# Kernel tuning notes

Hardware: AMD Instinct MI355X
Metric: run time of the kernel (lower is better)

## Reference

```python
import jax, jax.numpy as jnp
import numpy as np
import math

# Model hyperparameters (SchNet defaults)
H = 128        # hidden_channels
F = 128        # num_filters
G = 50         # num_gaussians
CUT = 6.0      # cutoff (Angstrom)
L_INT = 3      # num_interactions
# Graph scale
N_MOL = 512    # molecules
APM = 32       # atoms per molecule
N = N_MOL * APM
BOX = 10.0     # side of cubic box per molecule


def _ssp(x):
    # ShiftedSoftplus
    return jax.nn.softplus(x) - math.log(2.0)


def setup_inputs() -> dict:
    rng = np.random.default_rng(0)
    pos = rng.uniform(0.0, BOX, (N_MOL, APM, 3)).astype(np.float32)
    # radius graph within each molecule (faithful to radius_graph_custom,
    # precomputed here because edge count is data-dependent)
    srcs, dsts = [], []
    for m in range(N_MOL):
        p = pos[m]
        dm = np.linalg.norm(p[:, None, :] - p[None, :, :], axis=-1)
        mask = dm <= CUT
        np.fill_diagonal(mask, False)
        s, t = np.nonzero(mask)
        srcs.append(s + m * APM)
        dsts.append(t + m * APM)
    edge_index = np.stack([np.concatenate(srcs), np.concatenate(dsts)]).astype(np.int32)
    pos = pos.reshape(N, 3)
    batch = np.repeat(np.arange(N_MOL, dtype=np.int32), APM)
    z = rng.integers(1, 100, N).astype(np.int32)

    key = jax.random.key(0)
    ks = jax.random.split(key, 16)
    s = 0.1
    nrm = lambda k, shp: (jax.random.normal(k, shp, dtype=jnp.float32) * s)
    return {
        "z": jnp.asarray(z),
        "pos": jnp.asarray(pos),
        "batch": jnp.asarray(batch),
        "edge_index": jnp.asarray(edge_index),
        "emb": nrm(ks[0], (100, H)),
        "mlp_w1": nrm(ks[1], (L_INT, G, F)),
        "mlp_b1": jnp.zeros((L_INT, F), jnp.float32),
        "mlp_w2": nrm(ks[2], (L_INT, F, F)),
        "mlp_b2": jnp.zeros((L_INT, F), jnp.float32),
        "cf1_w": nrm(ks[3], (L_INT, H, F)),
        "cf2_w": nrm(ks[4], (L_INT, F, H)),
        "cf2_b": jnp.zeros((L_INT, H), jnp.float32),
        "lin_w": nrm(ks[5], (L_INT, H, H)),
        "lin_b": jnp.zeros((L_INT, H), jnp.float32),
        "out1_w": nrm(ks[6], (H, H // 2)),
        "out1_b": jnp.zeros((H // 2,), jnp.float32),
        "out2_w": nrm(ks[7], (H // 2, 1)),
        "out2_b": jnp.zeros((1,), jnp.float32),
    }


def reference(z, pos, batch, edge_index, emb,
              mlp_w1, mlp_b1, mlp_w2, mlp_b2,
              cf1_w, cf2_w, cf2_b, lin_w, lin_b,
              out1_w, out1_b, out2_w, out2_b):
    src, dst = edge_index[0], edge_index[1]
    # edge_weight = euclidean distance (== cdist[src, dst])
    d = jnp.sqrt(jnp.sum((pos[src] - pos[dst]) ** 2, axis=-1))  # [E]
    # GaussianSmearing
    offs = jnp.linspace(0.0, CUT, G)
    coeff = -0.5 / (CUT / (G - 1)) ** 2
    edge_attr = jnp.exp(coeff * (d[:, None] - offs[None, :]) ** 2)  # [E, G]
    # cosine cutoff
    Ccut = 0.5 * (jnp.cos(d * math.pi / CUT) + 1.0)  # [E]

    h = emb[z]  # [N, H]
    for l in range(L_INT):
        # edge filter MLP with cutoff
        W = _ssp(edge_attr @ mlp_w1[l] + mlp_b1[l]) @ mlp_w2[l] + mlp_b2[l]  # [E, F]
        W = W * Ccut[:, None]
        # CFConv: lin1 -> gather x_j -> multiply -> scatter-add to dst -> lin2
        msg = (h @ cf1_w[l])[src] * W                                # [E, F]
        agg = jax.ops.segment_sum(msg, dst, num_segments=N)          # [N, F]
        v = agg @ cf2_w[l] + cf2_b[l]                                # [N, H]
        v = _ssp(v)
        v = v @ lin_w[l] + lin_b[l]
        h = h + v  # residual

    h = _ssp(h @ out1_w + out1_b)
    h = h @ out2_w + out2_b                                          # [N, 1]
    out = jax.ops.segment_sum(h, batch, num_segments=N_MOL)          # [N_MOL, 1]
    return out
```

## Files before the change

### kernel.cpp

```cpp
#include <hip/hip_runtime.h>
#include <hip/hip_bf16.h>
#include <math.h>

#define NATOMS 16384
#define NMOL   512
#define APM    32
#define GDIM   50
#define KTAB   4096

#define STRH 132
#define STRA 136

typedef __attribute__((ext_vector_type(8))) short   short8;
typedef __attribute__((ext_vector_type(4))) float   floatx4;

__device__ __forceinline__ float ssp(float x) {
    float e = __expf(-fabsf(x));
    return fmaxf(x, 0.0f) + __logf(1.0f + e) - 0.69314718055994531f;
}

__device__ __forceinline__ unsigned short f2bf(float x) {
    union { float f; unsigned int u; } v; v.f = x;
    unsigned int lsb = (v.u >> 16) & 1u;
    v.u += 0x7fffu + lsb;
    return (unsigned short)(v.u >> 16);
}

__device__ __forceinline__ unsigned int pk2bf(float a, float b) {
    __hip_bfloat162 h = __float22bfloat162_rn(make_float2(a, b));
    unsigned int u;
    __builtin_memcpy(&u, &h, 4);
    return u;
}

#define KW1 72
#define KW2 136
#define NTILE (KTAB / 64)

__global__ __launch_bounds__(256) void mega_setup_kernel(
    const float* __restrict__ pos, const int* __restrict__ eidx, int E, int EB,
    int* __restrict__ rowptr,
    const float* __restrict__ cf1, const float* __restrict__ cf2,
    const float* __restrict__ lin, const float* __restrict__ out1,
    unsigned short* __restrict__ Wtall, unsigned int* __restrict__ meta,
    const float* __restrict__ w1_, const float* __restrict__ b1_,
    const float* __restrict__ w2_, const float* __restrict__ b2_,
    unsigned short* __restrict__ Tt)
{
    const int WB = (9 * 16384 + 64 * 128 + 255) / 256;
    const int b = blockIdx.x;
    const int tid = threadIdx.x;

    if (b < EB) {
        int idx = b * 256 + tid;
        if (idx < E) {
            int s = eidx[idx], t = eidx[E + idx];
            float dx = pos[3 * s]     - pos[3 * t];
            float dy = pos[3 * s + 1] - pos[3 * t + 1];
            float dz = pos[3 * s + 2] - pos[3 * t + 2];
            float d  = sqrtf(dx * dx + dy * dy + dz * dz);
            float u  = d * (float)(KTAB - 1) / 6.0f;
            int i = min((int)(u + 0.5f), KTAB - 1);
            meta[idx] = ((unsigned)i << 10) | ((unsigned)(s & 31) << 5) | (unsigned)(t & 31);
        } else if (idx < E + NATOMS + 1) {
            int a = idx - E;
            int lo = 0, hi = E;
            while (lo < hi) { int mid = (lo + hi) >> 1; if (eidx[mid] < a) lo = mid + 1; else hi = mid; }
            rowptr[a] = lo;
        } else if (idx < E + NATOMS + 1 + 3 * 128) {
            int q = idx - (E + NATOMS + 1);
            int l = q >> 7, f = q & 127;
            Tt[(size_t)l * (KTAB + 1) * 128 + (size_t)KTAB * 128 + f] = 0;
        }
        return;
    }
    if (b < EB + WB) {
        int idx = (b - EB) * 256 + tid;
        if (idx < 9 * 16384) {
            int wi = idx >> 14, rem = idx & 16383;
            int n = rem >> 7, k = rem & 127;
            int l = wi / 3, which = wi % 3;
            const float* src = (which == 0) ? cf1 : (which == 1) ? cf2 : lin;
            Wtall[idx] = f2bf(src[(size_t)l * 16384 + k * 128 + n]);
        } else if (idx < 9 * 16384 + 64 * 128) {
            int q = idx - 9 * 16384;
            int n = q >> 7, k = q & 127;
            Wtall[idx] = f2bf(out1[k * 64 + n]);
        }
        return;
    }

    __shared__ unsigned short s_bufA[128 * KW2];
    __shared__ unsigned short s_bufB[128 * KW1];

    const int tt = b - EB - WB;
    const int l  = tt / NTILE;
    const int bx = tt % NTILE;
    const float* w1 = w1_ + (size_t)l * GDIM * 128;
    const float* b1 = b1_ + (size_t)l * 128;
    const float* w2 = w2_ + (size_t)l * 128 * 128;
    const float* b2 = b2_ + (size_t)l * 128;
    unsigned short* Tg = Tt + (size_t)l * (KTAB + 1) * 128;

    unsigned short* s_w1T = s_bufB;
    unsigned short* s_w2T = s_bufA;
    unsigned short* s_t   = s_bufB;

    for (int i = tid; i < GDIM * 128; i += 256) {
        int g = i >> 7, f = i & 127;
        s_w1T[f * KW1 + g] = f2bf(w1[i]);
    }
    for (int i = tid; i < (64 - GDIM) * 128; i += 256) {
        int g = GDIM + (i >> 7), f = i & 127;
        s_w1T[f * KW1 + g] = 0;
    }
    for (int i = tid; i < 128 * 128; i += 256) {
        int k = i >> 7, n = i & 127;
        s_w2T[n * KW2 + k] = f2bf(w2[i]);
    }

    const int lane = tid & 63;
    const int w    = tid >> 6;
    const int l15  = lane & 15;
    const int quad = lane >> 4;

    float b1v[8], b2v[8];
    #pragma unroll
    for (int nt = 0; nt < 8; nt++) {
        b1v[nt] = b1[nt * 16 + l15];
        b2v[nt] = b2[nt * 16 + l15];
    }
    __syncthreads();

    const float hstep = 6.0f / (float)(KTAB - 1);
    const float step  = 6.0f / 49.0f;
    const float coeff = -0.5f / (step * step);
    const float pioc  = 3.14159265358979323846f / 6.0f;
    const int k0 = bx * 64;
    const float dm = (float)(k0 + w * 16 + l15) * hstep;

    floatx4 acc1[8];
    #pragma unroll
    for (int nt = 0; nt < 8; nt++) acc1[nt] = (floatx4){0.f, 0.f, 0.f, 0.f};
    #pragma unroll
    for (int ks = 0; ks < 2; ks++) {
        unsigned int ap[4];
        #pragma unroll
        for (int jj = 0; jj < 4; jj++) {
            int g0 = ks * 32 + quad * 8 + 2 * jj;
            float d0 = dm - (float)g0 * step;
            float d1 = dm - (float)(g0 + 1) * step;
            float v0 = (g0 < GDIM)     ? __expf(coeff * d0 * d0) : 0.0f;
            float v1 = (g0 + 1 < GDIM) ? __expf(coeff * d1 * d1) : 0.0f;
            ap[jj] = pk2bf(v0, v1);
        }
        short8 af;
        __builtin_memcpy(&af, ap, 16);
        #pragma unroll
        for (int nt = 0; nt < 8; nt++) {
            short8 bfg = *(const short8*)&s_w1T[(nt * 16 + l15) * KW1 + ks * 32 + quad * 8];
            acc1[nt] = __builtin_amdgcn_mfma_f32_16x16x32_bf16(af, bfg, acc1[nt], 0, 0, 0);
        }
    }
    __syncthreads();

    #pragma unroll
    for (int nt = 0; nt < 8; nt++) {
        #pragma unroll
        for (int r = 0; r < 4; r++) {
            int row = w * 16 + quad * 4 + r;
            s_t[row * KW2 + nt * 16 + l15] = f2bf(ssp(acc1[nt][r] + b1v[nt]));
        }
    }

    floatx4 acc2[8];
    #pragma unroll
    for (int nt = 0; nt < 8; nt++) acc2[nt] = (floatx4){0.f, 0.f, 0.f, 0.f};
    #pragma unroll
    for (int ks = 0; ks < 4; ks++) {
        short8 af = *(const short8*)&s_t[(w * 16 + l15) * KW2 + ks * 32 + quad * 8];
        #pragma unroll
        for (int nt = 0; nt < 8; nt++) {
            short8 bfg = *(const short8*)&s_w2T[(nt * 16 + l15) * KW2 + ks * 32 + quad * 8];
            acc2[nt] = __builtin_amdgcn_mfma_f32_16x16x32_bf16(af, bfg, acc2[nt], 0, 0, 0);
        }
    }

    #pragma unroll
    for (int nt = 0; nt < 8; nt++) {
        #pragma unroll
        for (int r = 0; r < 4; r++) {
            int row = w * 16 + quad * 4 + r;
            float d = (float)(k0 + row) * hstep;
            float cut = 0.5f * (__cosf(d * pioc) + 1.0f);
            Tg[(size_t)(k0 + row) * 128 + nt * 16 + l15] = f2bf((acc2[nt][r] + b2v[nt]) * cut);
        }
    }
}

__global__ __launch_bounds__(512, 4) void fused_schnet_kernel(
    const int* __restrict__ z, const float* __restrict__ emb,
    const int* __restrict__ rowptr, const unsigned int* __restrict__ meta,
    const unsigned short* __restrict__ Tt,
    const unsigned short* __restrict__ Wtall,
    const float* __restrict__ cf2_b, const float* __restrict__ lin_b,
    const float* __restrict__ out1_b, const float* __restrict__ out2_w,
    const float* __restrict__ out2_b,
    float* __restrict__ out)
{
    __shared__ float s_h[32 * STRH];
    __shared__ float s_hx[32 * 128];
    __shared__ unsigned short s_agg[32 * STRA];
    __shared__ unsigned int s_ko[32 * 32];
    __shared__ float s_red;
    unsigned short* s_t = (unsigned short*)s_hx;

    const int tid  = threadIdx.x;
    const int lane = tid & 63;
    const int w    = tid >> 6;
    const int l15  = lane & 15;
    const int quad = lane >> 4;
    const int r16  = (w & 1) * 16;
    const int c32  = (w >> 1) * 32;
    const int B0   = blockIdx.x * 32;

    const int half = lane >> 5;
    const int l31  = lane & 31;
    const unsigned tOff = (unsigned)(l31 << 3);
    const unsigned hOff = (unsigned)(l31 << 4);

    for (int i = tid; i < 32 * 128; i += 512) {
        int row = i >> 7, col = i & 127;
        s_h[row * STRH + col] = emb[(size_t)z[B0 + row] * 128 + col];
    }
    if (tid == 0) s_red = 0.0f;
    for (int i = tid; i < 32 * 32; i += 512)
        s_ko[i] = (unsigned)(KTAB << 8);

    const int ebase = rowptr[B0];
    const int nE    = rowptr[B0 + 32] - ebase;

    __syncthreads();

    for (int i = tid; i < nE; i += 512) {
        unsigned q = meta[ebase + i];
        int dstA = q & 31, srcA = (q >> 5) & 31;
        s_ko[(dstA << 5) + ((srcA & 1) << 4) + (srcA >> 1)] = (q >> 10) << 8;
    }

    const unsigned short* WtO = Wtall + 9 * 16384;
    const char* hxB = (const char*)s_hx;

    for (int l = 0; l < 3; l++) {
        const unsigned short* W1 = Wtall + (size_t)(l * 3 + 0) * 16384;
        const unsigned short* W2 = Wtall + (size_t)(l * 3 + 1) * 16384;
        const unsigned short* W3 = Wtall + (size_t)(l * 3 + 2) * 16384;
        const char* TlB = (const char*)(Tt + (size_t)l * (KTAB + 1) * 128);

        __syncthreads();

        floatx4 acc[2];
        #pragma unroll
        for (int nt = 0; nt < 2; nt++) acc[nt] = (floatx4){0.f, 0.f, 0.f, 0.f};
        #pragma unroll
        for (int ks = 0; ks < 4; ks++) {
            const float* hp = &s_h[(r16 + l15) * STRH + ks * 32 + quad * 8];
            float4 xa = *(const float4*)hp;
            float4 xb = *(const float4*)(hp + 4);
            unsigned int ap[4];
            ap[0] = pk2bf(xa.x, xa.y); ap[1] = pk2bf(xa.z, xa.w);
            ap[2] = pk2bf(xb.x, xb.y); ap[3] = pk2bf(xb.z, xb.w);
            short8 af;
            __builtin_memcpy(&af, ap, 16);
            #pragma unroll
            for (int nt = 0; nt < 2; nt++) {
                short8 bfg = *(const short8*)&W1[(size_t)(c32 + nt * 16 + l15) * 128 + ks * 32 + quad * 8];
                acc[nt] = __builtin_amdgcn_mfma_f32_16x16x32_bf16(af, bfg, acc[nt], 0, 0, 0);
            }
        }
        #pragma unroll
        for (int nt = 0; nt < 2; nt++) {
            #pragma unroll
            for (int r = 0; r < 4; r++)
                s_hx[(r16 + quad * 4 + r) * 128 + c32 + nt * 16 + l15] = acc[nt][r];
        }

        __syncthreads();

        for (int al = 0; al < 4; al++) {
            const int atom = (w << 2) + al;
            const unsigned* ko = &s_ko[(atom << 5) + (half << 4)];
            uint4 k0 = *(const uint4*)&ko[0];
            uint4 k1 = *(const uint4*)&ko[4];
            uint4 k2 = *(const uint4*)&ko[8];
            uint4 k3 = *(const uint4*)&ko[12];
            const unsigned koff[16] = { k0.x, k0.y, k0.z, k0.w,
                                        k1.x, k1.y, k1.z, k1.w,
                                        k2.x, k2.y, k2.z, k2.w,
                                        k3.x, k3.y, k3.z, k3.w };
            float pa[4][4];
            #pragma unroll
            for (int j = 0; j < 4; j++) {
                #pragma unroll
                for (int c = 0; c < 4; c++) pa[j][c] = 0.0f;
            }
            #pragma unroll
            for (int stp = 0; stp < 16; stp++) {
                const int pr = (stp << 1) + half;
                uint2 tp = *(const uint2*)(TlB + (koff[stp] + tOff));
                float4 hv = *(const float4*)(hxB + (unsigned)(pr << 9) + hOff);
                const int j = stp & 3;
                pa[j][0] = fmaf(hv.x, __uint_as_float(tp.x << 16),         pa[j][0]);
                pa[j][1] = fmaf(hv.y, __uint_as_float(tp.x & 0xffff0000u), pa[j][1]);
                pa[j][2] = fmaf(hv.z, __uint_as_float(tp.y << 16),         pa[j][2]);
                pa[j][3] = fmaf(hv.w, __uint_as_float(tp.y & 0xffff0000u), pa[j][3]);
            }
            float c0 = (pa[0][0] + pa[1][0]) + (pa[2][0] + pa[3][0]);
            float c1 = (pa[0][1] + pa[1][1]) + (pa[2][1] + pa[3][1]);
            float c2 = (pa[0][2] + pa[1][2]) + (pa[2][2] + pa[3][2]);
            float c3 = (pa[0][3] + pa[1][3]) + (pa[2][3] + pa[3][3]);
            c0 += __shfl_xor(c0, 32);
            c1 += __shfl_xor(c1, 32);
            c2 += __shfl_xor(c2, 32);
            c3 += __shfl_xor(c3, 32);
            if (half == 0) {
                uint2 pk = make_uint2(pk2bf(c0, c1), pk2bf(c2, c3));
                *(uint2*)&s_agg[atom * STRA + (l31 << 2)] = pk;
            }
        }

        __syncthreads();

        float bva[2], bvb[2];
        #pragma unroll
        for (int nt = 0; nt < 2; nt++) {
            bva[nt] = cf2_b[l * 128 + c32 + nt * 16 + l15];
            bvb[nt] = lin_b[l * 128 + c32 + nt * 16 + l15];
        }
        #pragma unroll
        for (int nt = 0; nt < 2; nt++) acc[nt] = (floatx4){0.f, 0.f, 0.f, 0.f};
        #pragma unroll
        for (int ks = 0; ks < 4; ks++) {
            short8 af = *(const short8*)&s_agg[(r16 + l15) * STRA + ks * 32 + quad * 8];
            #pragma unroll
            for (int nt = 0; nt < 2; nt++) {
                short8 bfg = *(const short8*)&W2[(size_t)(c32 + nt * 16 + l15) * 128 + ks * 32 + quad * 8];
                acc[nt] = __builtin_amdgcn_mfma_f32_16x16x32_bf16(af, bfg, acc[nt], 0, 0, 0);
            }
        }
        #pragma unroll
        for (int nt = 0; nt < 2; nt++) {
            #pragma unroll
            for (int r = 0; r < 4; r++) {
                int row = r16 + quad * 4 + r;
                s_t[row * STRA + c32 + nt * 16 + l15] = f2bf(ssp(acc[nt][r] + bva[nt]));
            }
        }

        __syncthreads();

        #pragma unroll
        for (int nt = 0; nt < 2; nt++) acc[nt] = (floatx4){0.f, 0.f, 0.f, 0.f};
        #pragma unroll
        for (int ks = 0; ks < 4; ks++) {
            short8 af = *(const short8*)&s_t[(r16 + l15) * STRA + ks * 32 + quad * 8];
            #pragma unroll
            for (int nt = 0; nt < 2; nt++) {
                short8 bfg = *(const short8*)&W3[(size_t)(c32 + nt * 16 + l15) * 128 + ks * 32 + quad * 8];
                acc[nt] = __builtin_amdgcn_mfma_f32_16x16x32_bf16(af, bfg, acc[nt], 0, 0, 0);
            }
        }
        #pragma unroll
        for (int nt = 0; nt < 2; nt++) {
            #pragma unroll
            for (int r = 0; r < 4; r++) {
                int row = r16 + quad * 4 + r;
                s_h[row * STRH + c32 + nt * 16 + l15] += acc[nt][r] + bvb[nt];
            }
        }
    }

    __syncthreads();

    const int c16 = (w >> 1) * 16;
    floatx4 ha = (floatx4){0.f, 0.f, 0.f, 0.f};
    #pragma unroll
    for (int ks = 0; ks < 4; ks++) {
        const float* hp = &s_h[(r16 + l15) * STRH + ks * 32 + quad * 8];
        float4 xa = *(const float4*)hp;
        float4 xb = *(const float4*)(hp + 4);
        unsigned int ap[4];
        ap[0] = pk2bf(xa.x, xa.y); ap[1] = pk2bf(xa.z, xa.w);
        ap[2] = pk2bf(xb.x, xb.y); ap[3] = pk2bf(xb.z, xb.w);
        short8 af;
        __builtin_memcpy(&af, ap, 16);
        short8 bfg = *(const short8*)&WtO[(size_t)(c16 + l15) * 128 + ks * 32 + quad * 8];
        ha = __builtin_amdgcn_mfma_f32_16x16x32_bf16(af, bfg, ha, 0, 0, 0);
    }
    float part = 0.0f;
    {
        float b1o = out1_b[c16 + l15];
        float o2  = out2_w[c16 + l15];
        #pragma unroll
        for (int r = 0; r < 4; r++)
            part += ssp(ha[r] + b1o) * o2;
    }
    #pragma unroll
    for (int off = 32; off > 0; off >>= 1) part += __shfl_down(part, off);
    if (lane == 0) atomicAdd(&s_red, part);
    __syncthreads();
    if (tid == 0) out[blockIdx.x] = s_red + 32.0f * out2_b[0];
}

extern "C" void kernel_launch(void* const* d_in, const int* in_sizes, int n_in,
                              void* d_out, int out_size, void* d_ws, size_t ws_size,
                              hipStream_t stream)
{
    const int*   z      = (const int*)d_in[0];
    const float* pos    = (const float*)d_in[1];
    const int*   eidx   = (const int*)d_in[3];
    const float* emb    = (const float*)d_in[4];
    const float* mlp_w1 = (const float*)d_in[5];
    const float* mlp_b1 = (const float*)d_in[6];
    const float* mlp_w2 = (const float*)d_in[7];
    const float* mlp_b2 = (const float*)d_in[8];
    const float* cf1_w  = (const float*)d_in[9];
    const float* cf2_w  = (const float*)d_in[10];
    const float* cf2_b  = (const float*)d_in[11];
    const float* lin_w  = (const float*)d_in[12];
    const float* lin_b  = (const float*)d_in[13];
    const float* out1_w = (const float*)d_in[14];
    const float* out1_b = (const float*)d_in[15];
    const float* out2_w = (const float*)d_in[16];
    const float* out2_b = (const float*)d_in[17];
    const int E = in_sizes[3] / 2;

    char* p = (char*)d_ws;
    unsigned int* meta = (unsigned int*)p;        p += ((size_t)(E + 1) * 4 + 63) & ~63ULL;
    unsigned short* Tt = (unsigned short*)p;      p += (size_t)3 * (KTAB + 1) * 128 * 2;
    int* rowptr = (int*)p;                        p += ((size_t)(NATOMS + 1) * 4 + 63) & ~63ULL;
    unsigned short* Wtall = (unsigned short*)p;

    const int EB = (E + NATOMS + 1 + 3 * 128 + 255) / 256;
    const int WB = (9 * 16384 + 64 * 128 + 255) / 256;
    const int TB = NTILE * 3;
    mega_setup_kernel<<<EB + WB + TB, 256, 0, stream>>>(
        pos, eidx, E, EB, rowptr, cf1_w, cf2_w, lin_w, out1_w, Wtall, meta,
        mlp_w1, mlp_b1, mlp_w2, mlp_b2, Tt);

    fused_schnet_kernel<<<NMOL, 512, 0, stream>>>(
        z, emb, rowptr, meta, Tt, Wtall,
        cf2_b, lin_b, out1_b, out2_w, out2_b, (float*)d_out);
}
```

Before: 170.0 us.

## Restructure message aggregation so each lane owns two features across four atoms

The per-atom aggregation loop is rewritten. Each wave now handles its four destination atoms together, with each lane owning two feature columns instead of splitting sources across half-waves. Each source atom's h-row value is loaded once and reused for all four destination atoms. Table offsets are made wave-uniform via readfirstlane, which removes the cross-half shuffle reduction and the interleaved s_ko layout. In exchange, table loads become 4-byte per lane instead of 8-byte, and more register accumulators are live at once.

```diff
diff --git a/kernel.cpp b/kernel.cpp
--- a/kernel.cpp
+++ b/kernel.cpp
@@ -224,11 +224,6 @@
     const int c32  = (w >> 1) * 32;
     const int B0   = blockIdx.x * 32;
 
-    const int half = lane >> 5;
-    const int l31  = lane & 31;
-    const unsigned tOff = (unsigned)(l31 << 3);
-    const unsigned hOff = (unsigned)(l31 << 4);
-
     for (int i = tid; i < 32 * 128; i += 512) {
         int row = i >> 7, col = i & 127;
         s_h[row * STRH + col] = emb[(size_t)z[B0 + row] * 128 + col];
@@ -245,11 +240,10 @@
     for (int i = tid; i < nE; i += 512) {
         unsigned q = meta[ebase + i];
         int dstA = q & 31, srcA = (q >> 5) & 31;
-        s_ko[(dstA << 5) + ((srcA & 1) << 4) + (srcA >> 1)] = (q >> 10) << 8;
+        s_ko[(dstA << 5) + srcA] = (q >> 10) << 8;
     }
 
     const unsigned short* WtO = Wtall + 9 * 16384;
-    const char* hxB = (const char*)s_hx;
 
     for (int l = 0; l < 3; l++) {
         const unsigned short* W1 = Wtall + (size_t)(l * 3 + 0) * 16384;
@@ -287,46 +281,40 @@
 
         __syncthreads();
 
-        for (int al = 0; al < 4; al++) {
-            const int atom = (w << 2) + al;
-            const unsigned* ko = &s_ko[(atom << 5) + (half << 4)];
-            uint4 k0 = *(const uint4*)&ko[0];
-            uint4 k1 = *(const uint4*)&ko[4];
-            uint4 k2 = *(const uint4*)&ko[8];
-            uint4 k3 = *(const uint4*)&ko[12];
-            const unsigned koff[16] = { k0.x, k0.y, k0.z, k0.w,
-                                        k1.x, k1.y, k1.z, k1.w,
-                                        k2.x, k2.y, k2.z, k2.w,
-                                        k3.x, k3.y, k3.z, k3.w };
-            float pa[4][4];
-            #pragma unroll
-            for (int j = 0; j < 4; j++) {
+        {
+            float acc0[4], acc1[4];
+            #pragma unroll
+            for (int i = 0; i < 4; i++) { acc0[i] = 0.0f; acc1[i] = 0.0f; }
+            #pragma unroll
+            for (int sc = 0; sc < 4; sc++) {
+                unsigned ko[4][8];
                 #pragma unroll
-                for (int c = 0; c < 4; c++) pa[j][c] = 0.0f;
-            }
-            #pragma unroll
-            for (int stp = 0; stp < 16; stp++) {
-                const int pr = (stp << 1) + half;
-                uint2 tp = *(const uint2*)(TlB + (koff[stp] + tOff));
-                float4 hv = *(const float4*)(hxB + (unsigned)(pr << 9) + hOff);
-                const int j = stp & 3;
-                pa[j][0] = fmaf(hv.x, __uint_as_float(tp.x << 16),         pa[j][0]);
-                pa[j][1] = fmaf(hv.y, __uint_as_float(tp.x & 0xffff0000u), pa[j][1]);
-                pa[j][2] = fmaf(hv.z, __uint_as_float(tp.y << 16),         pa[j][2]);
-                pa[j][3] = fmaf(hv.w, __uint_as_float(tp.y & 0xffff0000u), pa[j][3]);
-            }
-            float c0 = (pa[0][0] + pa[1][0]) + (pa[2][0] + pa[3][0]);
-            float c1 = (pa[0][1] + pa[1][1]) + (pa[2][1] + pa[3][1]);
-            float c2 = (pa[0][2] + pa[1][2]) + (pa[2][2] + pa[3][2]);
-            float c3 = (pa[0][3] + pa[1][3]) + (pa[2][3] + pa[3][3]);
-            c0 += __shfl_xor(c0, 32);
-            c1 += __shfl_xor(c1, 32);
-            c2 += __shfl_xor(c2, 32);
-            c3 += __shfl_xor(c3, 32);
-            if (half == 0) {
-                uint2 pk = make_uint2(pk2bf(c0, c1), pk2bf(c2, c3));
-                *(uint2*)&s_agg[atom * STRA + (l31 << 2)] = pk;
-            }
+                for (int i = 0; i < 4; i++) {
+                    uint4 ka = *(const uint4*)&s_ko[(((w << 2) + i) << 5) + (sc << 3)];
+                    uint4 kb = *(const uint4*)&s_ko[(((w << 2) + i) << 5) + (sc << 3) + 4];
+                    ko[i][0] = __builtin_amdgcn_readfirstlane(ka.x);
+                    ko[i][1] = __builtin_amdgcn_readfirstlane(ka.y);
+                    ko[i][2] = __builtin_amdgcn_readfirstlane(ka.z);
+                    ko[i][3] = __builtin_amdgcn_readfirstlane(ka.w);
+                    ko[i][4] = __builtin_amdgcn_readfirstlane(kb.x);
+                    ko[i][5] = __builtin_amdgcn_readfirstlane(kb.y);
+                    ko[i][6] = __builtin_amdgcn_readfirstlane(kb.z);
+                    ko[i][7] = __builtin_amdgcn_readfirstlane(kb.w);
+                }
+                #pragma unroll
+                for (int j = 0; j < 8; j++) {
+                    float2 hv = *(const float2*)&s_hx[(((sc << 3) + j) << 7) + (lane << 1)];
+                    #pragma unroll
+                    for (int i = 0; i < 4; i++) {
+                        unsigned tp = *(const unsigned*)(TlB + ko[i][j] + (unsigned)(lane << 2));
+                        acc0[i] = fmaf(hv.x, __uint_as_float(tp << 16),         acc0[i]);
+                        acc1[i] = fmaf(hv.y, __uint_as_float(tp & 0xffff0000u), acc1[i]);
+                    }
+                }
+            }
+            #pragma unroll
+            for (int i = 0; i < 4; i++)
+                *(unsigned*)&s_agg[(((w << 2) + i)) * STRA + (lane << 1)] = pk2bf(acc0[i], acc1[i]);
         }
 
         __syncthreads();
```

Result: faster. 161.2 us (-5.1%).
